# Kernel optimization log

Measured on AMD Instinct MI355X. Metric: run time of the kernel, lower is better.

The kernel has to match this reference:

```python
import jax, jax.numpy as jnp
import numpy as np

B, C, H, W = 256, 512, 14, 14  # C = rnn_size
S = 7                          # spp_size

def setup_inputs() -> dict:
    key = jax.random.key(0)
    ks = jax.random.split(key, 8)
    sd = 1.0 / np.sqrt(C)
    return {
        "att_v": jax.random.normal(ks[0], (B, C, H, W), dtype=jnp.float32),
        "h": jax.random.normal(ks[1], (B, C), dtype=jnp.float32),
        # a2a: Linear(rnn_size, rnn_size)
        "Wa": jax.random.uniform(ks[2], (C, C), jnp.float32, -sd, sd),
        "ba": jax.random.uniform(ks[3], (C,), jnp.float32, -sd, sd),
        # h2a: Linear(rnn_size, rnn_size)
        "Wh": jax.random.uniform(ks[4], (C, C), jnp.float32, -sd, sd),
        "bh": jax.random.uniform(ks[5], (C,), jnp.float32, -sd, sd),
        # d2d: Linear(rnn_size, 1)
        "Wd": jax.random.uniform(ks[6], (C,), jnp.float32, -sd, sd),
        "bd": jax.random.uniform(ks[7], (1,), jnp.float32, -sd, sd),
    }

def reference(att_v, h, Wa, ba, Wh, bh, Wd, bd):
    b, c, hh, ww = att_v.shape
    # AdaptiveAvgPool2d(S) with H,W divisible by S -> block mean
    pooled = att_v.reshape(b, c, S, hh // S, S, ww // S).mean(axis=(3, 5))  # [B,C,S,S]
    a = pooled.reshape(b, c, S * S).transpose(0, 2, 1)  # [B, N=49, C]
    av = jnp.einsum('bnc,dc->bnd', a, Wa) + ba          # a2a, torch Linear: x @ W.T + b
    ah = h @ Wh.T + bh                                  # h2a, [B,C]
    dot = jnp.tanh(av + ah[:, None, :])                 # broadcast add + tanh
    scores = jnp.einsum('bnd,d->bn', dot, Wd) + bd[0]   # d2d -> [B, N]
    weight = jax.nn.softmax(scores, axis=-1)            # over attention positions
    att_res = jnp.einsum('bnc,bn->bc', a, weight)       # bmm(att^T, weight)
    return att_res
```

## Files before the change

kernel.cpp:

```cpp
#include <hip/hip_runtime.h>
#include <hip/hip_bf16.h>

#define BATCH 256
#define CDIM  512
#define NPOS  49
#define NPAD  64
#define ASTRIDE 520

typedef __attribute__((ext_vector_type(8))) short bf16x8_t;
typedef __attribute__((ext_vector_type(4))) float f32x4_t;

__global__ void prep_convert(const float* __restrict__ Wa,
                             const float* __restrict__ Wh,
                             __hip_bfloat16* __restrict__ Wab,
                             __hip_bfloat16* __restrict__ Whb) {
    int gid = blockIdx.x * blockDim.x + threadIdx.x;
    const int quarter = (CDIM * CDIM) / 4;
    const float4* src;
    __hip_bfloat16* dst;
    int idx;
    if (gid < quarter) { src = (const float4*)Wa; dst = Wab; idx = gid; }
    else               { src = (const float4*)Wh; dst = Whb; idx = gid - quarter; }
    float4 v = src[idx];
    dst[idx * 4 + 0] = __float2bfloat16(v.x);
    dst[idx * 4 + 1] = __float2bfloat16(v.y);
    dst[idx * 4 + 2] = __float2bfloat16(v.z);
    dst[idx * 4 + 3] = __float2bfloat16(v.w);
}

__global__ __launch_bounds__(512, 2) void att_spp_main(
    const float* __restrict__ att_v,
    const float* __restrict__ h,
    const float* __restrict__ ba,
    const float* __restrict__ bh,
    const float* __restrict__ Wd,
    const __hip_bfloat16* __restrict__ Wab,
    const __hip_bfloat16* __restrict__ Whb,
    float* __restrict__ out)
{
    __shared__ __hip_bfloat16 a_lds[NPAD * ASTRIDE];
    __shared__ __hip_bfloat16 h_lds[CDIM];
    __shared__ float babh_lds[CDIM];
    __shared__ float wd_lds[CDIM];
    __shared__ float scores_lds[NPAD];
    __shared__ float weights_lds[NPOS];

    const int b = blockIdx.x;
    const int t = threadIdx.x;

    h_lds[t]    = __float2bfloat16(h[b * CDIM + t]);
    babh_lds[t] = ba[t] + bh[t];
    wd_lds[t]   = Wd[t];
    if (t < NPAD) scores_lds[t] = 0.f;
    for (int idx = t; idx < (NPAD - NPOS) * ASTRIDE; idx += 512)
        a_lds[NPOS * ASTRIDE + idx] = __float2bfloat16(0.f);

    {
        const int jj = t & 7;
        const int g  = t >> 3;
        const float2* att2 = (const float2*)(att_v + (size_t)b * CDIM * 196);
        if (jj < 7) {
            for (int ci = 0; ci < 8; ++ci) {
                const int c = g + (ci << 6);
                const int cbase = c * 98;
                #pragma unroll
                for (int i = 0; i < 7; ++i) {
                    float2 v0 = att2[cbase + i * 14 + jj];
                    float2 v1 = att2[cbase + i * 14 + 7 + jj];
                    float p = (v0.x + v0.y + v1.x + v1.y) * 0.25f;
                    a_lds[(i * 7 + jj) * ASTRIDE + c] = __float2bfloat16(p);
                }
            }
        }
    }
    __syncthreads();

    const int wave = t >> 6;
    const int lane = t & 63;
    const int q = lane >> 4;
    const int r = lane & 15;

    f32x4_t acc[4][4];
    #pragma unroll
    for (int rt = 0; rt < 4; ++rt)
        #pragma unroll
        for (int ct = 0; ct < 4; ++ct)
            acc[rt][ct] = (f32x4_t){0.f, 0.f, 0.f, 0.f};

    const int dBase = wave * 64 + r;

    for (int ks = 0; ks < 16; ++ks) {
        const int k0 = ks * 32 + q * 8;
        bf16x8_t af[4];
        #pragma unroll
        for (int rt = 0; rt < 4; ++rt)
            af[rt] = *(const bf16x8_t*)&a_lds[(rt * 16 + r) * ASTRIDE + k0];
        bf16x8_t bf[4];
        #pragma unroll
        for (int ct = 0; ct < 4; ++ct)
            bf[ct] = *(const bf16x8_t*)&Wab[(size_t)(dBase + ct * 16) * CDIM + k0];
        #pragma unroll
        for (int rt = 0; rt < 4; ++rt)
            #pragma unroll
            for (int ct = 0; ct < 4; ++ct)
                acc[rt][ct] = __builtin_amdgcn_mfma_f32_16x16x32_bf16(
                    af[rt], bf[ct], acc[rt][ct], 0, 0, 0);
    }
    for (int ks = 0; ks < 16; ++ks) {
        const int k0 = ks * 32 + q * 8;
        bf16x8_t af = *(const bf16x8_t*)&h_lds[k0];
        bf16x8_t bf[4];
        #pragma unroll
        for (int ct = 0; ct < 4; ++ct)
            bf[ct] = *(const bf16x8_t*)&Whb[(size_t)(dBase + ct * 16) * CDIM + k0];
        #pragma unroll
        for (int rt = 0; rt < 4; ++rt)
            #pragma unroll
            for (int ct = 0; ct < 4; ++ct)
                acc[rt][ct] = __builtin_amdgcn_mfma_f32_16x16x32_bf16(
                    af, bf[ct], acc[rt][ct], 0, 0, 0);
    }

    float part[4][4];
    #pragma unroll
    for (int rt = 0; rt < 4; ++rt)
        #pragma unroll
        for (int rg = 0; rg < 4; ++rg) part[rt][rg] = 0.f;

    #pragma unroll
    for (int ct = 0; ct < 4; ++ct) {
        const int d = dBase + ct * 16;
        const float bias = babh_lds[d];
        const float wd = wd_lds[d];
        #pragma unroll
        for (int rt = 0; rt < 4; ++rt)
            #pragma unroll
            for (int rg = 0; rg < 4; ++rg) {
                float x = acc[rt][ct][rg] + bias;
                float e = __expf(2.f * x);
                part[rt][rg] += (1.f - 2.f / (e + 1.f)) * wd;
            }
    }
    #pragma unroll
    for (int m = 1; m < 16; m <<= 1)
        #pragma unroll
        for (int rt = 0; rt < 4; ++rt)
            #pragma unroll
            for (int rg = 0; rg < 4; ++rg)
                part[rt][rg] += __shfl_xor(part[rt][rg], m, 64);
    if (r == 0) {
        #pragma unroll
        for (int rt = 0; rt < 4; ++rt)
            #pragma unroll
            for (int rg = 0; rg < 4; ++rg)
                atomicAdd(&scores_lds[rt * 16 + q * 4 + rg], part[rt][rg]);
    }
    __syncthreads();

    if (wave == 0) {
        float v = (lane < NPOS) ? scores_lds[lane] : -3.0e38f;
        float vmax = v;
        #pragma unroll
        for (int m = 1; m < 64; m <<= 1)
            vmax = fmaxf(vmax, __shfl_xor(vmax, m, 64));
        float e = (lane < NPOS) ? __expf(v - vmax) : 0.f;
        float s = e;
        #pragma unroll
        for (int m = 1; m < 64; m <<= 1)
            s += __shfl_xor(s, m, 64);
        if (lane < NPOS) weights_lds[lane] = e / s;
    }
    __syncthreads();

    {
        float sum = 0.f;
        #pragma unroll
        for (int n = 0; n < NPOS; ++n)
            sum += __bfloat162float(a_lds[n * ASTRIDE + t]) * weights_lds[n];
        out[b * CDIM + t] = sum;
    }
}

extern "C" void kernel_launch(void* const* d_in, const int* in_sizes, int n_in,
                              void* d_out, int out_size, void* d_ws, size_t ws_size,
                              hipStream_t stream) {
    const float* att_v = (const float*)d_in[0];
    const float* h     = (const float*)d_in[1];
    const float* Wa    = (const float*)d_in[2];
    const float* ba    = (const float*)d_in[3];
    const float* Wh    = (const float*)d_in[4];
    const float* bh    = (const float*)d_in[5];
    const float* Wd    = (const float*)d_in[6];

    __hip_bfloat16* Wab = (__hip_bfloat16*)d_ws;
    __hip_bfloat16* Whb = Wab + (size_t)CDIM * CDIM;

    prep_convert<<<512, 256, 0, stream>>>(Wa, Wh, Wab, Whb);
    att_spp_main<<<BATCH, 512, 0, stream>>>(att_v, h, ba, bh, Wd, Wab, Whb,
                                            (float*)d_out);
}
```

Measured before the change: 201.8 us.

## Split fused attention kernel into pool, GEMM-score, and softmax-wsum kernels

Replaces the single per-batch fused kernel (256 blocks) with a four-kernel pipeline: a prep kernel converts the weights and h to bf16 and zeroes the scores, a pool kernel stages att_v through LDS with coalesced float4 loads, a GEMM kernel splits the output dimension four ways (1024 blocks) and accumulates scores with global atomics, and a final kernel does the softmax and weighted sum. The aim is more parallelism and better occupancy than 256 large blocks, plus coalesced reads of att_v. In exchange it adds extra launches, a pooled bf16 intermediate written to and read back from global memory, and float atomics that make the score sums order-nondeterministic. The old path remains as a fallback when the workspace is too small.

New measurement: 233.7 us. +15.8%, slower.

```diff
diff --git a/kernel.cpp b/kernel.cpp
--- a/kernel.cpp
+++ b/kernel.cpp
@@ -9,6 +9,186 @@
 
 typedef __attribute__((ext_vector_type(8))) short bf16x8_t;
 typedef __attribute__((ext_vector_type(4))) float f32x4_t;
+
+#define WS_NEED 18153472u
+
+__global__ __launch_bounds__(256) void prep(
+    const float* __restrict__ Wa, const float* __restrict__ Wh,
+    const float* __restrict__ h,
+    __hip_bfloat16* __restrict__ Wab, __hip_bfloat16* __restrict__ Whb,
+    __hip_bfloat16* __restrict__ hb, float* __restrict__ scores) {
+    int gid = blockIdx.x * 256 + threadIdx.x;
+    if (gid < 163840) {
+        const float* src; __hip_bfloat16* dst; int idx;
+        if (gid < 65536)       { src = Wa; dst = Wab; idx = gid; }
+        else if (gid < 131072) { src = Wh; dst = Whb; idx = gid - 65536; }
+        else                   { src = h;  dst = hb;  idx = gid - 131072; }
+        float4 v = ((const float4*)src)[idx];
+        dst[idx * 4 + 0] = __float2bfloat16(v.x);
+        dst[idx * 4 + 1] = __float2bfloat16(v.y);
+        dst[idx * 4 + 2] = __float2bfloat16(v.z);
+        dst[idx * 4 + 3] = __float2bfloat16(v.w);
+    } else {
+        int idx = gid - 163840;
+        ((float4*)scores)[idx] = (float4){0.f, 0.f, 0.f, 0.f};
+    }
+}
+
+__global__ __launch_bounds__(256, 6) void pool_kernel(
+    const float* __restrict__ att_v, __hip_bfloat16* __restrict__ pooled) {
+    __shared__ float4 lds[32 * 49];
+    const int b  = blockIdx.x >> 4;
+    const int cg = blockIdx.x & 15;
+    const int t  = threadIdx.x;
+
+    const float4* src = (const float4*)(att_v + ((size_t)b * CDIM + cg * 32) * 196);
+    #pragma unroll
+    for (int k = 0; k < 7; ++k) {
+        int idx = t + k * 256;
+        if (idx < 1568) lds[idx] = src[idx];
+    }
+    __syncthreads();
+
+    const int i = t >> 5;
+    const int c = t & 31;
+    if (i < 7) {
+        const float4* fp = &lds[c * 49 + 7 * i];
+        float4 f0 = fp[0], f1 = fp[1], f2 = fp[2], f3 = fp[3];
+        float4 f4 = fp[4], f5 = fp[5], f6 = fp[6];
+        float p[7];
+        p[0] = f0.x + f0.y + f3.z + f3.w;
+        p[1] = f0.z + f0.w + f4.x + f4.y;
+        p[2] = f1.x + f1.y + f4.z + f4.w;
+        p[3] = f1.z + f1.w + f5.x + f5.y;
+        p[4] = f2.x + f2.y + f5.z + f5.w;
+        p[5] = f2.z + f2.w + f6.x + f6.y;
+        p[6] = f3.x + f3.y + f6.z + f6.w;
+        __hip_bfloat16* outp = pooled + (size_t)b * NPAD * CDIM + cg * 32 + c;
+        #pragma unroll
+        for (int j = 0; j < 7; ++j)
+            outp[(size_t)(i * 7 + j) * CDIM] = __float2bfloat16(p[j] * 0.25f);
+    }
+}
+
+__global__ __launch_bounds__(256, 4) void gemm_score(
+    const __hip_bfloat16* __restrict__ pooled,
+    const __hip_bfloat16* __restrict__ Wab,
+    const __hip_bfloat16* __restrict__ Whb,
+    const __hip_bfloat16* __restrict__ hb,
+    const float* __restrict__ ba, const float* __restrict__ bh,
+    const float* __restrict__ Wd, float* __restrict__ scores) {
+    __shared__ float s_lds[NPAD];
+    const int b    = blockIdx.x >> 2;
+    const int jt   = blockIdx.x & 3;
+    const int wave = threadIdx.x >> 6;
+    const int lane = threadIdx.x & 63;
+    const int q = lane >> 4;
+    const int r = lane & 15;
+
+    if (threadIdx.x < NPAD) s_lds[threadIdx.x] = 0.f;
+
+    const int d0 = jt * 128 + wave * 32 + r;
+    const __hip_bfloat16* Ap = pooled + (size_t)b * NPAD * CDIM;
+    const __hip_bfloat16* hp = hb + (size_t)b * CDIM;
+
+    f32x4_t acc[4][2];
+    #pragma unroll
+    for (int rt = 0; rt < 4; ++rt)
+        #pragma unroll
+        for (int ct = 0; ct < 2; ++ct)
+            acc[rt][ct] = (f32x4_t){0.f, 0.f, 0.f, 0.f};
+
+    #pragma unroll 4
+    for (int ks = 0; ks < 16; ++ks) {
+        const int k0 = ks * 32 + q * 8;
+        bf16x8_t af[4], bf[2];
+        #pragma unroll
+        for (int rt = 0; rt < 4; ++rt)
+            af[rt] = *(const bf16x8_t*)&Ap[(size_t)(rt * 16 + r) * CDIM + k0];
+        #pragma unroll
+        for (int ct = 0; ct < 2; ++ct)
+            bf[ct] = *(const bf16x8_t*)&Wab[(size_t)(d0 + 16 * ct) * CDIM + k0];
+        #pragma unroll
+        for (int rt = 0; rt < 4; ++rt)
+            #pragma unroll
+            for (int ct = 0; ct < 2; ++ct)
+                acc[rt][ct] = __builtin_amdgcn_mfma_f32_16x16x32_bf16(
+                    af[rt], bf[ct], acc[rt][ct], 0, 0, 0);
+    }
+    #pragma unroll 4
+    for (int ks = 0; ks < 16; ++ks) {
+        const int k0 = ks * 32 + q * 8;
+        bf16x8_t ah = *(const bf16x8_t*)&hp[k0];
+        bf16x8_t bf[2];
+        #pragma unroll
+        for (int ct = 0; ct < 2; ++ct)
+            bf[ct] = *(const bf16x8_t*)&Whb[(size_t)(d0 + 16 * ct) * CDIM + k0];
+        #pragma unroll
+        for (int rt = 0; rt < 4; ++rt)
+            #pragma unroll
+            for (int ct = 0; ct < 2; ++ct)
+                acc[rt][ct] = __builtin_amdgcn_mfma_f32_16x16x32_bf16(
+                    ah, bf[ct], acc[rt][ct], 0, 0, 0);
+    }
+
+    float part[4][4];
+    #pragma unroll
+    for (int rt = 0; rt < 4; ++rt)
+        #pragma unroll
+        for (int rg = 0; rg < 4; ++rg) part[rt][rg] = 0.f;
+    #pragma unroll
+    for (int ct = 0; ct < 2; ++ct) {
+        const int d = d0 + 16 * ct;
+        const float bias = ba[d] + bh[d];
+        const float wd = Wd[d];
+        #pragma unroll
+        for (int rt = 0; rt < 4; ++rt)
+            #pragma unroll
+            for (int rg = 0; rg < 4; ++rg) {
+                float x = acc[rt][ct][rg] + bias;
+                float e = __expf(2.f * x);
+                part[rt][rg] += (1.f - 2.f / (e + 1.f)) * wd;
+            }
+    }
+    #pragma unroll
+    for (int m = 1; m < 16; m <<= 1)
+        #pragma unroll
+        for (int rt = 0; rt < 4; ++rt)
+            #pragma unroll
+            for (int rg = 0; rg < 4; ++rg)
+                part[rt][rg] += __shfl_xor(part[rt][rg], m, 64);
+    __syncthreads();
+    if (r == 0) {
+        #pragma unroll
+        for (int rt = 0; rt < 4; ++rt)
+            #pragma unroll
+            for (int rg = 0; rg < 4; ++rg)
+                atomicAdd(&s_lds[rt * 16 + q * 4 + rg], part[rt][rg]);
+    }
+    __syncthreads();
+    if (threadIdx.x < NPAD)
+        atomicAdd(&scores[b * NPAD + threadIdx.x], s_lds[threadIdx.x]);
+}
+
+__global__ __launch_bounds__(256) void softmax_wsum(
+    const float* __restrict__ scores, const __hip_bfloat16* __restrict__ pooled,
+    float* __restrict__ out) {
+    const int b  = blockIdx.x >> 1;
+    const int ch = (blockIdx.x & 1) * 256 + threadIdx.x;
+    const float* sp = scores + b * NPAD;
+    float vmax = -3.0e38f;
+    #pragma unroll
+    for (int n = 0; n < NPOS; ++n) vmax = fmaxf(vmax, sp[n]);
+    const __hip_bfloat16* Ap = pooled + (size_t)b * NPAD * CDIM + ch;
+    float sum = 0.f, accv = 0.f;
+    #pragma unroll
+    for (int n = 0; n < NPOS; ++n) {
+        float e = __expf(sp[n] - vmax);
+        sum += e;
+        accv += e * __bfloat162float(Ap[(size_t)n * CDIM]);
+    }
+    out[b * CDIM + ch] = accv / sum;
+}
 
 __global__ void prep_convert(const float* __restrict__ Wa,
                              const float* __restrict__ Wh,
@@ -16,9 +196,7 @@
                              __hip_bfloat16* __restrict__ Whb) {
     int gid = blockIdx.x * blockDim.x + threadIdx.x;
     const int quarter = (CDIM * CDIM) / 4;
-    const float4* src;
-    __hip_bfloat16* dst;
-    int idx;
+    const float4* src; __hip_bfloat16* dst; int idx;
     if (gid < quarter) { src = (const float4*)Wa; dst = Wab; idx = gid; }
     else               { src = (const float4*)Wh; dst = Whb; idx = gid - quarter; }
     float4 v = src[idx];
@@ -29,73 +207,54 @@
 }
 
 __global__ __launch_bounds__(512, 2) void att_spp_main(
-    const float* __restrict__ att_v,
-    const float* __restrict__ h,
-    const float* __restrict__ ba,
-    const float* __restrict__ bh,
+    const float* __restrict__ att_v, const float* __restrict__ h,
+    const float* __restrict__ ba, const float* __restrict__ bh,
     const float* __restrict__ Wd,
-    const __hip_bfloat16* __restrict__ Wab,
-    const __hip_bfloat16* __restrict__ Whb,
-    float* __restrict__ out)
-{
+    const __hip_bfloat16* __restrict__ Wab, const __hip_bfloat16* __restrict__ Whb,
+    float* __restrict__ out) {
     __shared__ __hip_bfloat16 a_lds[NPAD * ASTRIDE];
     __shared__ __hip_bfloat16 h_lds[CDIM];
     __shared__ float babh_lds[CDIM];
     __shared__ float wd_lds[CDIM];
     __shared__ float scores_lds[NPAD];
     __shared__ float weights_lds[NPOS];
-
-    const int b = blockIdx.x;
-    const int t = threadIdx.x;
-
+    const int b = blockIdx.x, t = threadIdx.x;
     h_lds[t]    = __float2bfloat16(h[b * CDIM + t]);
     babh_lds[t] = ba[t] + bh[t];
     wd_lds[t]   = Wd[t];
     if (t < NPAD) scores_lds[t] = 0.f;
     for (int idx = t; idx < (NPAD - NPOS) * ASTRIDE; idx += 512)
         a_lds[NPOS * ASTRIDE + idx] = __float2bfloat16(0.f);
-
     {
-        const int jj = t & 7;
-        const int g  = t >> 3;
+        const int jj = t & 7, g = t >> 3;
         const float2* att2 = (const float2*)(att_v + (size_t)b * CDIM * 196);
         if (jj < 7) {
             for (int ci = 0; ci < 8; ++ci) {
-                const int c = g + (ci << 6);
-                const int cbase = c * 98;
+                const int c = g + (ci << 6), cbase = c * 98;
                 #pragma unroll
                 for (int i = 0; i < 7; ++i) {
                     float2 v0 = att2[cbase + i * 14 + jj];
                     float2 v1 = att2[cbase + i * 14 + 7 + jj];
-                    float p = (v0.x + v0.y + v1.x + v1.y) * 0.25f;
-                    a_lds[(i * 7 + jj) * ASTRIDE + c] = __float2bfloat16(p);
+                    a_lds[(i * 7 + jj) * ASTRIDE + c] =
+                        __float2bfloat16((v0.x + v0.y + v1.x + v1.y) * 0.25f);
                 }
             }
         }
     }
     __syncthreads();
-
-    const int wave = t >> 6;
-    const int lane = t & 63;
-    const int q = lane >> 4;
-    const int r = lane & 15;
-
+    const int wave = t >> 6, lane = t & 63, q = lane >> 4, r = lane & 15;
     f32x4_t acc[4][4];
     #pragma unroll
     for (int rt = 0; rt < 4; ++rt)
         #pragma unroll
-        for (int ct = 0; ct < 4; ++ct)
-            acc[rt][ct] = (f32x4_t){0.f, 0.f, 0.f, 0.f};
-
+        for (int ct = 0; ct < 4; ++ct) acc[rt][ct] = (f32x4_t){0.f,0.f,0.f,0.f};
     const int dBase = wave * 64 + r;
-
     for (int ks = 0; ks < 16; ++ks) {
         const int k0 = ks * 32 + q * 8;
-        bf16x8_t af[4];
+        bf16x8_t af[4], bf[4];
         #pragma unroll
         for (int rt = 0; rt < 4; ++rt)
             af[rt] = *(const bf16x8_t*)&a_lds[(rt * 16 + r) * ASTRIDE + k0];
-        bf16x8_t bf[4];
         #pragma unroll
         for (int ct = 0; ct < 4; ++ct)
             bf[ct] = *(const bf16x8_t*)&Wab[(size_t)(dBase + ct * 16) * CDIM + k0];
@@ -120,18 +279,15 @@
                 acc[rt][ct] = __builtin_amdgcn_mfma_f32_16x16x32_bf16(
                     af, bf[ct], acc[rt][ct], 0, 0, 0);
     }
-
     float part[4][4];
     #pragma unroll
     for (int rt = 0; rt < 4; ++rt)
         #pragma unroll
         for (int rg = 0; rg < 4; ++rg) part[rt][rg] = 0.f;
-
     #pragma unroll
     for (int ct = 0; ct < 4; ++ct) {
         const int d = dBase + ct * 16;
-        const float bias = babh_lds[d];
-        const float wd = wd_lds[d];
+        const float bias = babh_lds[d], wd = wd_lds[d];
         #pragma unroll
         for (int rt = 0; rt < 4; ++rt)
             #pragma unroll
@@ -156,29 +312,23 @@
                 atomicAdd(&scores_lds[rt * 16 + q * 4 + rg], part[rt][rg]);
     }
     __syncthreads();
-
     if (wave == 0) {
         float v = (lane < NPOS) ? scores_lds[lane] : -3.0e38f;
         float vmax = v;
         #pragma unroll
-        for (int m = 1; m < 64; m <<= 1)
-            vmax = fmaxf(vmax, __shfl_xor(vmax, m, 64));
+        for (int m = 1; m < 64; m <<= 1) vmax = fmaxf(vmax, __shfl_xor(vmax, m, 64));
         float e = (lane < NPOS) ? __expf(v - vmax) : 0.f;
         float s = e;
         #pragma unroll
-        for (int m = 1; m < 64; m <<= 1)
-            s += __shfl_xor(s, m, 64);
+        for (int m = 1; m < 64; m <<= 1) s += __shfl_xor(s, m, 64);
         if (lane < NPOS) weights_lds[lane] = e / s;
     }
     __syncthreads();
-
-    {
-        float sum = 0.f;
-        #pragma unroll
-        for (int n = 0; n < NPOS; ++n)
-            sum += __bfloat162float(a_lds[n * ASTRIDE + t]) * weights_lds[n];
-        out[b * CDIM + t] = sum;
-    }
+    float sum = 0.f;
+    #pragma unroll
+    for (int n = 0; n < NPOS; ++n)
+        sum += __bfloat162float(a_lds[n * ASTRIDE + t]) * weights_lds[n];
+    out[b * CDIM + t] = sum;
 }
 
 extern "C" void kernel_launch(void* const* d_in, const int* in_sizes, int n_in,
@@ -192,10 +342,23 @@
     const float* bh    = (const float*)d_in[5];
     const float* Wd    = (const float*)d_in[6];
 
-    __hip_bfloat16* Wab = (__hip_bfloat16*)d_ws;
-    __hip_bfloat16* Whb = Wab + (size_t)CDIM * CDIM;
-
-    prep_convert<<<512, 256, 0, stream>>>(Wa, Wh, Wab, Whb);
-    att_spp_main<<<BATCH, 512, 0, stream>>>(att_v, h, ba, bh, Wd, Wab, Whb,
-                                            (float*)d_out);
-}
+    if (ws_size >= WS_NEED) {
+        char* ws = (char*)d_ws;
+        __hip_bfloat16* Wab    = (__hip_bfloat16*)(ws);
+        __hip_bfloat16* Whb    = (__hip_bfloat16*)(ws + 524288);
+        __hip_bfloat16* hb     = (__hip_bfloat16*)(ws + 1048576);
+        __hip_bfloat16* pooled = (__hip_bfloat16*)(ws + 1310720);
+        float*          scores = (float*)(ws + 18087936);
+
+        prep<<<656, 256, 0, stream>>>(Wa, Wh, h, Wab, Whb, hb, scores);
+        pool_kernel<<<4096, 256, 0, stream>>>(att_v, pooled);
+        gemm_score<<<1024, 256, 0, stream>>>(pooled, Wab, Whb, hb, ba, bh, Wd, scores);
+        softmax_wsum<<<512, 256, 0, stream>>>(scores, pooled, (float*)d_out);
+    } else {
+        __hip_bfloat16* Wab = (__hip_bfloat16*)d_ws;
+        __hip_bfloat16* Whb = Wab + (size_t)CDIM * CDIM;
+        prep_convert<<<512, 256, 0, stream>>>(Wa, Wh, Wab, Whb);
+        att_spp_main<<<BATCH, 512, 0, stream>>>(att_v, h, ba, bh, Wd, Wab, Whb,
+                                                (float*)d_out);
+    }
+}
```
